# Kernel optimization log

Hardware: AMD Instinct MI355X
Metric: run time of the kernel (lower is better)

## Reference

```python
import jax, jax.numpy as jnp
import numpy as np

B, D, C, P = 64, 262144, 4, 4096  # batch, original_dim, c, proj_dim


def setup_inputs() -> dict:
    key = jax.random.key(0)
    kx, ki, ks = jax.random.split(key, 3)
    x = jax.random.normal(kx, (B, D), dtype=jnp.float32)
    rand_indices = jax.random.randint(ki, (D, C), 0, P, dtype=jnp.int64)
    rand_sign_bits = jax.random.randint(ks, (D, C), 0, 2, dtype=jnp.int32)
    return {"x": x, "rand_indices": rand_indices, "rand_sign_bits": rand_sign_bits}


def reference(x, rand_indices, rand_sign_bits):
    # signs in {-1, +1}, matching (randint(0,2)*2 - 1) in the torch module
    signs = (2 * rand_sign_bits - 1).astype(x.dtype)          # [D, C]
    idx = rand_indices.reshape(-1)                             # [D*C]
    vals = (x[:, :, None] * signs[None, :, :]).reshape(x.shape[0], -1)  # [B, D*C]
    # scatter-add each signed value into its hashed projection slot
    project = lambda v: jax.ops.segment_sum(v, idx, num_segments=P)
    return jax.vmap(project)(vals)                             # [B, P]
```

## Files before the change

### kernel.cpp

```cpp
#include <hip/hip_runtime.h>
#include <hip/hip_bf16.h>
#include <hip/hip_fp16.h>


constexpr int B_DIM = 64;
constexpr int D_DIM = 262144;
constexpr int P_DIM = 4096;

constexpr int NDS   = 64;
constexpr int SLICE = D_DIM / NDS;
constexpr int NBIN  = 16;
constexpr int NSC   = 16;
constexpr int SC_D  = SLICE / NSC;
constexpr int BCAP  = 128;
constexpr int NHB   = 32;
constexpr int G_DS  = 4;
constexpr int NDG   = NDS / G_DS;
constexpr int WPB   = 8;
constexpr int PR_W  = 16;
constexpr int NPR   = P_DIM / PR_W;
constexpr int LCAP  = 128;

constexpr size_t REG_OFF   = 0;
constexpr size_t REG_BYTES = (size_t)NDS * NSC * NBIN * BCAP * 4;
constexpr size_t CNT_OFF   = REG_OFF + REG_BYTES;
constexpr size_t CNT_BYTES = (size_t)NDS * NSC * NBIN * 4;
constexpr size_t XT_OFF    = CNT_OFF + CNT_BYTES;
constexpr size_t XT_BYTES  = (size_t)D_DIM * B_DIM * 2;
constexpr size_t PART_OFF  = XT_OFF + XT_BYTES;
constexpr size_t PART_BYTES = (size_t)NPR * NDG * PR_W * B_DIM * 2;
constexpr size_t WS_NEED   = PART_OFF + PART_BYTES;

__global__ __launch_bounds__(256) void k_binpack(
    const int* __restrict__ idx, const int* __restrict__ sgn,
    unsigned* __restrict__ reg, int* __restrict__ cnt) {
    const int w = threadIdx.x >> 6, lane = threadIdx.x & 63;
    const int dslice  = blockIdx.x >> 2;
    const int quarter = blockIdx.x & 3;
    const int sc      = quarter * 4 + w;
    const int d0      = dslice * SLICE + sc * SC_D;
    unsigned* regw = reg + ((size_t)(dslice * NSC + sc) * NBIN) * BCAP;
    const unsigned long long lmask = (1ull << lane) - 1ull;

    unsigned cb[16];
    #pragma unroll
    for (int b = 0; b < 16; ++b) cb[b] = 0;

    #pragma unroll
    for (int step = 0; step < SC_D / 64; ++step) {
        const int dli = step * 64 + lane;
        const int4 iv = reinterpret_cast<const int4*>(idx)[d0 + dli];
        const int4 sv = reinterpret_cast<const int4*>(sgn)[d0 + dli];
        const unsigned rowbyte = (unsigned)((sc * SC_D + dli) << 7);
        #pragma unroll
        for (int c = 0; c < 4; ++c) {
            const unsigned p = ((unsigned)((c==0)?iv.x:(c==1)?iv.y:(c==2)?iv.z:iv.w)) & 4095u;
            const unsigned s = ((unsigned)((c==0)?sv.x:(c==1)?sv.y:(c==2)?sv.z:sv.w)) & 1u;
            const unsigned e = rowbyte | ((p & 255u) << 19) | ((s ^ 1u) << 31);
            const unsigned bin = p >> 8;
            unsigned pos = 0;
            #pragma unroll
            for (int b = 0; b < 16; ++b) {
                const unsigned long long m = __ballot(bin == (unsigned)b);
                if (bin == (unsigned)b) pos = cb[b] + (unsigned)__popcll(m & lmask);
                cb[b] += (unsigned)__popcll(m);
            }
            if (pos < (unsigned)BCAP) regw[bin * BCAP + pos] = e;
        }
    }
    unsigned cval = 0;
    #pragma unroll
    for (int b = 0; b < 16; ++b) {
        const unsigned cc = cb[b] < (unsigned)BCAP ? cb[b] : (unsigned)BCAP;
        cval = (lane == b) ? cc : cval;
    }
    if (lane < 16) cnt[(dslice * NSC + sc) * NBIN + lane] = (int)cval;
}

__global__ __launch_bounds__(256) void k_transpose(
    const float* __restrict__ x, unsigned short* __restrict__ xTh) {
    __shared__ float tile[64 * 65];
    const int d0 = blockIdx.x * 64;
    const int t = threadIdx.x;
    const int lane = t & 63;
    #pragma unroll
    for (int k = 0; k < 16; ++k) {
        const int b = k * 4 + (t >> 6);
        tile[lane * 65 + b] = x[(size_t)b * D_DIM + d0 + lane];
    }
    __syncthreads();
    #pragma unroll
    for (int k = 0; k < 16; ++k) {
        const int dr = k * 4 + (t >> 6);
        const __half h = __float2half_rn(tile[dr * 65 + lane]);
        xTh[(size_t)(d0 + dr) * B_DIM + lane] = __builtin_bit_cast(unsigned short, h);
    }
}

__global__ __launch_bounds__(512, 8) void k_process(
    const unsigned* __restrict__ reg, const int* __restrict__ cnt,
    const unsigned short* __restrict__ xTh, __half* __restrict__ part) {
    __shared__ __half2 hist[WPB][2 * PR_W * 32];
    __shared__ unsigned lst[WPB][LCAP];
    __shared__ int cnts[WPB][WPB];
    __shared__ int baseL[WPB][WPB];
    __shared__ int totals[WPB];

    const int w = threadIdx.x >> 6, lane = threadIdx.x & 63;
    const int dg  = blockIdx.x & 15;
    const int hb  = blockIdx.x >> 4;
    const int bin = hb >> 1, half = hb & 1;

    __half2* hw = hist[w];
    {
        unsigned* h32 = reinterpret_cast<unsigned*>(hw);
        #pragma unroll
        for (int k = 0; k < 16; ++k) h32[k * 64 + lane] = 0u;
    }

    const unsigned long long lmask = (1ull << lane) - 1ull;
    const unsigned li4 = (unsigned)(lane & 31) * 4u;
    const bool hi = lane >= 32;
    const unsigned l31 = (unsigned)(lane & 31);

    for (int ds = 0; ds < G_DS; ++ds) {
        const int dslice = dg * G_DS + ds;

        unsigned er[4];
        int n0 = 0, n1 = 0;
        int c0 = 0, c1 = 0, c2 = 0, c3 = 0, c4 = 0, c5 = 0, c6 = 0, c7 = 0;
        #pragma unroll
        for (int sc2 = 0; sc2 < 2; ++sc2) {
            const int sc = 2 * w + sc2;
            const int n  = cnt[(dslice * NSC + sc) * NBIN + bin];
            const unsigned* list = reg + ((size_t)((dslice * NSC + sc) * NBIN + bin)) * BCAP;
            if (sc2 == 0) n0 = n; else n1 = n;
            #pragma unroll
            for (int b = 0; b < 2; ++b) {
                const int i = b * 64 + lane;
                const unsigned e = (i < n) ? list[i] : 0u;
                er[sc2 * 2 + b] = e;
                const unsigned po8 = (e >> 19) & 255u;
                const bool valid = (i < n) && ((int)(po8 >> 7) == half);
                const unsigned t = valid ? ((po8 >> 4) & 7u) : 0xFFu;
                c0 += __popcll(__ballot(t == 0u)); c1 += __popcll(__ballot(t == 1u));
                c2 += __popcll(__ballot(t == 2u)); c3 += __popcll(__ballot(t == 3u));
                c4 += __popcll(__ballot(t == 4u)); c5 += __popcll(__ballot(t == 5u));
                c6 += __popcll(__ballot(t == 6u)); c7 += __popcll(__ballot(t == 7u));
            }
        }
        {
            int cval = 0;
            cval = (lane == 0) ? c0 : cval; cval = (lane == 1) ? c1 : cval;
            cval = (lane == 2) ? c2 : cval; cval = (lane == 3) ? c3 : cval;
            cval = (lane == 4) ? c4 : cval; cval = (lane == 5) ? c5 : cval;
            cval = (lane == 6) ? c6 : cval; cval = (lane == 7) ? c7 : cval;
            if (lane < 8) cnts[w][lane] = cval;
        }
        __syncthreads();

        if (w == 0 && lane < 8) {
            int run = 0;
            #pragma unroll
            for (int ww = 0; ww < 8; ++ww) { baseL[lane][ww] = run; run += cnts[ww][lane]; }
            totals[lane] = run;
        }
        __syncthreads();

        c0 = c1 = c2 = c3 = c4 = c5 = c6 = c7 = 0;
        #pragma unroll
        for (int sc2 = 0; sc2 < 2; ++sc2) {
            const int n = (sc2 == 0) ? n0 : n1;
            #pragma unroll
            for (int b = 0; b < 2; ++b) {
                const int i = b * 64 + lane;
                const unsigned e = er[sc2 * 2 + b];
                const unsigned po8 = (e >> 19) & 255u;
                const bool valid = (i < n) && ((int)(po8 >> 7) == half);
                const unsigned t = valid ? ((po8 >> 4) & 7u) : 0xFFu;
                const unsigned long long m0 = __ballot(t == 0u);
                const unsigned long long m1 = __ballot(t == 1u);
                const unsigned long long m2 = __ballot(t == 2u);
                const unsigned long long m3 = __ballot(t == 3u);
                const unsigned long long m4 = __ballot(t == 4u);
                const unsigned long long m5 = __ballot(t == 5u);
                const unsigned long long m6 = __ballot(t == 6u);
                const unsigned long long m7 = __ballot(t == 7u);
                if (valid) {
                    const unsigned long long mt =
                        t < 4u ? (t < 2u ? (t == 0u ? m0 : m1) : (t == 2u ? m2 : m3))
                               : (t < 6u ? (t == 4u ? m4 : m5) : (t == 6u ? m6 : m7));
                    const int cbase =
                        t < 4u ? (t < 2u ? (t == 0u ? c0 : c1) : (t == 2u ? c2 : c3))
                               : (t < 6u ? (t == 4u ? c4 : c5) : (t == 6u ? c6 : c7));
                    const int pos = baseL[t][w] + cbase + (int)__popcll(mt & lmask);
                    if (pos < LCAP) lst[t][pos] = e;
                }
                c0 += __popcll(m0); c1 += __popcll(m1);
                c2 += __popcll(m2); c3 += __popcll(m3);
                c4 += __popcll(m4); c5 += __popcll(m5);
                c6 += __popcll(m6); c7 += __popcll(m7);
            }
        }
        __syncthreads();

        const char* xs_c = reinterpret_cast<const char*>(xTh) + (size_t)dslice * SLICE * 128;
        const int n = totals[w] < LCAP ? totals[w] : LCAP;
        const unsigned* L = lst[w];

        int i = 0;
        for (; i + 8 <= n; i += 8) {
            const uint4 A  = *reinterpret_cast<const uint4*>(L + i);
            const uint4 Bv = *reinterpret_cast<const uint4*>(L + i + 4);
            const unsigned e0 = __builtin_amdgcn_readfirstlane(A.x);
            const unsigned e1 = __builtin_amdgcn_readfirstlane(A.y);
            const unsigned e2 = __builtin_amdgcn_readfirstlane(A.z);
            const unsigned e3 = __builtin_amdgcn_readfirstlane(A.w);
            const unsigned e4 = __builtin_amdgcn_readfirstlane(Bv.x);
            const unsigned e5 = __builtin_amdgcn_readfirstlane(Bv.y);
            const unsigned e6 = __builtin_amdgcn_readfirstlane(Bv.z);
            const unsigned e7 = __builtin_amdgcn_readfirstlane(Bv.w);
            const unsigned va0 = (hi ? (e4 & 0x7FFFFu) : (e0 & 0x7FFFFu)) + li4;
            const unsigned va1 = (hi ? (e5 & 0x7FFFFu) : (e1 & 0x7FFFFu)) + li4;
            const unsigned va2 = (hi ? (e6 & 0x7FFFFu) : (e2 & 0x7FFFFu)) + li4;
            const unsigned va3 = (hi ? (e7 & 0x7FFFFu) : (e3 & 0x7FFFFu)) + li4;
            const unsigned d0 = *reinterpret_cast<const unsigned*>(xs_c + va0);
            const unsigned d1 = *reinterpret_cast<const unsigned*>(xs_c + va1);
            const unsigned d2 = *reinterpret_cast<const unsigned*>(xs_c + va2);
            const unsigned d3 = *reinterpret_cast<const unsigned*>(xs_c + va3);

            const unsigned pL0 = (e0 >> 19) & 15u, pL1 = (e1 >> 19) & 15u;
            const unsigned pL2 = (e2 >> 19) & 15u, pL3 = (e3 >> 19) & 15u;
            const unsigned pH0 = (e4 >> 19) & 15u, pH1 = (e5 >> 19) & 15u;
            const unsigned pH2 = (e6 >> 19) & 15u, pH3 = (e7 >> 19) & 15u;

            __half2 v[4];
            #pragma unroll
            for (int k = 0; k < 4; ++k) {
                const unsigned dv = (k == 0) ? d0 : (k == 1) ? d1 : (k == 2) ? d2 : d3;
                const unsigned eL = (k == 0) ? e0 : (k == 1) ? e1 : (k == 2) ? e2 : e3;
                const unsigned eH = (k == 0) ? e4 : (k == 1) ? e5 : (k == 2) ? e6 : e7;
                const unsigned sm = hi ? (eH & 0x80000000u) : (eL & 0x80000000u);
                v[k] = __builtin_bit_cast(__half2, dv ^ (sm ? 0x80008000u : 0u));
            }

            const __half2 zero2 = __builtin_bit_cast(__half2, 0u);
            {
                const bool m01 = hi ? (pH0 == pH1) : (pL0 == pL1);
                v[1] = m01 ? __hadd2(v[1], v[0]) : v[1];  v[0] = m01 ? zero2 : v[0];
                const bool m02 = hi ? (pH0 == pH2) : (pL0 == pL2);
                v[2] = m02 ? __hadd2(v[2], v[0]) : v[2];  v[0] = m02 ? zero2 : v[0];
                const bool m12 = hi ? (pH1 == pH2) : (pL1 == pL2);
                v[2] = m12 ? __hadd2(v[2], v[1]) : v[2];  v[1] = m12 ? zero2 : v[1];
                const bool m03 = hi ? (pH0 == pH3) : (pL0 == pL3);
                v[3] = m03 ? __hadd2(v[3], v[0]) : v[3];  v[0] = m03 ? zero2 : v[0];
                const bool m13 = hi ? (pH1 == pH3) : (pL1 == pL3);
                v[3] = m13 ? __hadd2(v[3], v[1]) : v[3];  v[1] = m13 ? zero2 : v[1];
                const bool m23 = hi ? (pH2 == pH3) : (pL2 == pL3);
                v[3] = m23 ? __hadd2(v[3], v[2]) : v[3];  v[2] = m23 ? zero2 : v[2];
            }

            const unsigned a0 = (hi ? (512u + pH0 * 32u) : (pL0 * 32u)) + l31;
            const unsigned a1 = (hi ? (512u + pH1 * 32u) : (pL1 * 32u)) + l31;
            const unsigned a2 = (hi ? (512u + pH2 * 32u) : (pL2 * 32u)) + l31;
            const unsigned a3 = (hi ? (512u + pH3 * 32u) : (pL3 * 32u)) + l31;
            const __half2 h0 = hw[a0];
            const __half2 h1 = hw[a1];
            const __half2 h2v = hw[a2];
            const __half2 h3 = hw[a3];
            hw[a0] = __hadd2(h0, v[0]);
            hw[a1] = __hadd2(h1, v[1]);
            hw[a2] = __hadd2(h2v, v[2]);
            hw[a3] = __hadd2(h3, v[3]);
        }
        for (; i + 2 <= n; i += 2) {
            const unsigned eA = __builtin_amdgcn_readfirstlane(L[i]);
            const unsigned eB = __builtin_amdgcn_readfirstlane(L[i + 1]);
            const unsigned va = (hi ? (eB & 0x7FFFFu) : (eA & 0x7FFFFu)) + li4;
            const unsigned dv = *reinterpret_cast<const unsigned*>(xs_c + va);
            const unsigned sm = hi ? (eB & 0x80000000u) : (eA & 0x80000000u);
            const __half2 v2 = __builtin_bit_cast(__half2, dv ^ (sm ? 0x80008000u : 0u));
            const unsigned po = hi ? ((eB >> 19) & 15u) : ((eA >> 19) & 15u);
            const unsigned a = (hi ? (512u + po * 32u) : (po * 32u)) + l31;
            hw[a] = __hadd2(hw[a], v2);
        }
        if (i < n) {
            const unsigned eA = __builtin_amdgcn_readfirstlane(L[i]);
            if (!hi) {
                const unsigned va = (eA & 0x7FFFFu) + li4;
                const unsigned dv = *reinterpret_cast<const unsigned*>(xs_c + va);
                const __half2 v2 = __builtin_bit_cast(__half2,
                    dv ^ ((eA & 0x80000000u) ? 0x80008000u : 0u));
                const unsigned a = ((eA >> 19) & 15u) * 32u + l31;
                hw[a] = __hadd2(hw[a], v2);
            }
        }
        __syncthreads();
    }

    unsigned* wp32 = reinterpret_cast<unsigned*>(
        part + ((size_t)((hb * WPB + w) * NDG + dg)) * (PR_W * B_DIM));
    #pragma unroll
    for (int k = 0; k < 8; ++k) {
        const int idxw = k * 64 + lane;
        const __half2 s = __hadd2(hw[idxw], hw[512 + idxw]);
        wp32[idxw] = __builtin_bit_cast(unsigned, s);
    }
}

__global__ __launch_bounds__(256) void k_reduce(
    const __half* __restrict__ part, float* __restrict__ out) {
    const int pr = blockIdx.x;
    const int t  = threadIdx.x;

    float4 acc = make_float4(0.f, 0.f, 0.f, 0.f);
    const size_t base = (size_t)pr * NDG * (PR_W * B_DIM);
    for (int dgi = 0; dgi < NDG; ++dgi) {
        const uint2 pv = *reinterpret_cast<const uint2*>(
            part + base + (size_t)dgi * (PR_W * B_DIM) + t * 4);
        const __half2 h0 = __builtin_bit_cast(__half2, pv.x);
        const __half2 h1 = __builtin_bit_cast(__half2, pv.y);
        acc.x += __half2float(h0.x); acc.y += __half2float(h0.y);
        acc.z += __half2float(h1.x); acc.w += __half2float(h1.y);
    }

    __shared__ float st[16][65];
    const int po = (t * 4) >> 6;
    const int b0 = (t * 4) & 63;
    st[po][b0]     = acc.x; st[po][b0 + 1] = acc.y;
    st[po][b0 + 2] = acc.z; st[po][b0 + 3] = acc.w;
    __syncthreads();

    #pragma unroll
    for (int k = 0; k < 4; ++k) {
        const int flat = k * 256 + t;
        const int b = flat >> 4, poo = flat & 15;
        out[(size_t)b * P_DIM + pr * PR_W + poo] = st[poo][b];
    }
}

__device__ __forceinline__ float signed_val(float x, int s) {
    return __uint_as_float(__float_as_uint(x) ^ (((unsigned)(s ^ 1)) << 31));
}

__global__ __launch_bounds__(1024) void sjlt_hist_fb(
    const float* __restrict__ x, const int* __restrict__ idx,
    const int* __restrict__ sgn, float* __restrict__ out) {
    __shared__ float hist[2][P_DIM];
    for (int i = threadIdx.x; i < 2 * P_DIM; i += 1024) (&hist[0][0])[i] = 0.0f;
    __syncthreads();
    const int chunk = blockIdx.x, bg = blockIdx.y;
    const int d0 = chunk * (D_DIM / 16), b0 = bg * 2;
    const float* xr0 = x + (size_t)b0 * D_DIM + d0;
    const float* xr1 = xr0 + D_DIM;
    const int4* iv4 = reinterpret_cast<const int4*>(idx) + d0;
    const int4* sv4 = reinterpret_cast<const int4*>(sgn) + d0;
    for (int t = threadIdx.x; t < D_DIM / 16; t += 1024) {
        const int4 iv = iv4[t]; const int4 sv = sv4[t];
        const float x0 = xr0[t], x1 = xr1[t];
        unsafeAtomicAdd(&hist[0][iv.x], signed_val(x0, sv.x));
        unsafeAtomicAdd(&hist[0][iv.y], signed_val(x0, sv.y));
        unsafeAtomicAdd(&hist[0][iv.z], signed_val(x0, sv.z));
        unsafeAtomicAdd(&hist[0][iv.w], signed_val(x0, sv.w));
        unsafeAtomicAdd(&hist[1][iv.x], signed_val(x1, sv.x));
        unsafeAtomicAdd(&hist[1][iv.y], signed_val(x1, sv.y));
        unsafeAtomicAdd(&hist[1][iv.z], signed_val(x1, sv.z));
        unsafeAtomicAdd(&hist[1][iv.w], signed_val(x1, sv.w));
    }
    __syncthreads();
    float* o = out + (size_t)b0 * P_DIM;
    for (int p = threadIdx.x; p < P_DIM; p += 1024) {
        unsafeAtomicAdd(&o[p],         hist[0][p]);
        unsafeAtomicAdd(&o[P_DIM + p], hist[1][p]);
    }
}

extern "C" void kernel_launch(void* const* d_in, const int* in_sizes, int n_in,
                              void* d_out, int out_size, void* d_ws, size_t ws_size,
                              hipStream_t stream) {
    const float* x   = (const float*)d_in[0];
    const int*   idx = (const int*)d_in[1];
    const int*   sgn = (const int*)d_in[2];
    float* out = (float*)d_out;

    if (ws_size >= WS_NEED) {
        char* ws = (char*)d_ws;
        unsigned* reg = (unsigned*)(ws + REG_OFF);
        int* cnt      = (int*)(ws + CNT_OFF);
        unsigned short* xTh = (unsigned short*)(ws + XT_OFF);
        __half* part  = (__half*)(ws + PART_OFF);

        k_binpack<<<NDS * 4, 256, 0, stream>>>(idx, sgn, reg, cnt);
        k_transpose<<<D_DIM / 64, 256, 0, stream>>>(x, xTh);
        k_process<<<NHB * NDG, 512, 0, stream>>>(reg, cnt, xTh, part);
        k_reduce<<<NPR, 256, 0, stream>>>(part, out);
    } else {
        hipMemsetAsync(d_out, 0, (size_t)out_size * sizeof(float), stream);
        dim3 grid(16, 32);
        sjlt_hist_fb<<<grid, 1024, 0, stream>>>(x, idx, sgn, out);
    }
}
```

Measured before the change: 78.50 us.

## Accumulate projection bins in registers per lane instead of shared-memory histograms

The process kernel drops the per-wave shared-memory half2 histogram and the block-wide prefix-sum list compaction. Each wave now builds small per-subchunk queues of packed 16-bit entries, and each lane accumulates one batch element's 16 projection outputs in scalar half registers, reading one half per entry. The d-slice grouping is halved and the block index mapping is reordered. This removes shared-memory read-modify-write traffic and two block barriers per slice. In exchange it adds branchy register selection and lower per-load width, and it silently truncates entries beyond 24 per queue.

```diff
diff --git a/kernel.cpp b/kernel.cpp
--- a/kernel.cpp
+++ b/kernel.cpp
@@ -14,12 +14,12 @@
 constexpr int SC_D  = SLICE / NSC;
 constexpr int BCAP  = 128;
 constexpr int NHB   = 32;
-constexpr int G_DS  = 4;
+constexpr int G_DS  = 2;
 constexpr int NDG   = NDS / G_DS;
 constexpr int WPB   = 8;
 constexpr int PR_W  = 16;
 constexpr int NPR   = P_DIM / PR_W;
-constexpr int LCAP  = 128;
+constexpr int QCAP  = 28;
 
 constexpr size_t REG_OFF   = 0;
 constexpr size_t REG_BYTES = (size_t)NDS * NSC * NBIN * BCAP * 4;
@@ -100,84 +100,58 @@
 __global__ __launch_bounds__(512, 8) void k_process(
     const unsigned* __restrict__ reg, const int* __restrict__ cnt,
     const unsigned short* __restrict__ xTh, __half* __restrict__ part) {
-    __shared__ __half2 hist[WPB][2 * PR_W * 32];
-    __shared__ unsigned lst[WPB][LCAP];
-    __shared__ int cnts[WPB][WPB];
-    __shared__ int baseL[WPB][WPB];
-    __shared__ int totals[WPB];
+    __shared__ unsigned short q[WPB][NSC][QCAP];
+    __shared__ short qcnt[WPB][NSC];
 
     const int w = threadIdx.x >> 6, lane = threadIdx.x & 63;
-    const int dg  = blockIdx.x & 15;
-    const int hb  = blockIdx.x >> 4;
+    const int dg  = blockIdx.x >> 5;
+    const int hb  = blockIdx.x & 31;
     const int bin = hb >> 1, half = hb & 1;
-
-    __half2* hw = hist[w];
-    {
-        unsigned* h32 = reinterpret_cast<unsigned*>(hw);
-        #pragma unroll
-        for (int k = 0; k < 16; ++k) h32[k * 64 + lane] = 0u;
-    }
-
     const unsigned long long lmask = (1ull << lane) - 1ull;
-    const unsigned li4 = (unsigned)(lane & 31) * 4u;
-    const bool hi = lane >= 32;
-    const unsigned l31 = (unsigned)(lane & 31);
-
-    for (int ds = 0; ds < G_DS; ++ds) {
-        const int dslice = dg * G_DS + ds;
-
-        unsigned er[4];
-        int n0 = 0, n1 = 0;
-        int c0 = 0, c1 = 0, c2 = 0, c3 = 0, c4 = 0, c5 = 0, c6 = 0, c7 = 0;
+    const int lane2 = lane * 2;
+
+    __half a0{}, a1{}, a2{}, a3{}, a4{}, a5{}, a6{}, a7{};
+    __half a8{}, a9{}, a10{}, a11{}, a12{}, a13{}, a14{}, a15{};
+
+    auto ADD = [&](unsigned e, unsigned short u) {
+        if (!(e & 0x4000u)) {
+            const unsigned short uv = u ^ (unsigned short)(e & 0x8000u);
+            const __half hv = __builtin_bit_cast(__half, uv);
+            const unsigned po = (e >> 8) & 15u;
+            if (po < 8u) {
+                if (po < 4u) {
+                    if (po < 2u) { if (po == 0u) a0 = __hadd(a0, hv); else a1 = __hadd(a1, hv); }
+                    else         { if (po == 2u) a2 = __hadd(a2, hv); else a3 = __hadd(a3, hv); }
+                } else {
+                    if (po < 6u) { if (po == 4u) a4 = __hadd(a4, hv); else a5 = __hadd(a5, hv); }
+                    else         { if (po == 6u) a6 = __hadd(a6, hv); else a7 = __hadd(a7, hv); }
+                }
+            } else {
+                if (po < 12u) {
+                    if (po < 10u) { if (po == 8u)  a8 = __hadd(a8, hv);  else a9 = __hadd(a9, hv); }
+                    else          { if (po == 10u) a10 = __hadd(a10, hv); else a11 = __hadd(a11, hv); }
+                } else {
+                    if (po < 14u) { if (po == 12u) a12 = __hadd(a12, hv); else a13 = __hadd(a13, hv); }
+                    else          { if (po == 14u) a14 = __hadd(a14, hv); else a15 = __hadd(a15, hv); }
+                }
+            }
+        }
+    };
+
+    for (int ds_i = 0; ds_i < G_DS; ++ds_i) {
+        const int dslice = dg * G_DS + ds_i;
+
         #pragma unroll
         for (int sc2 = 0; sc2 < 2; ++sc2) {
             const int sc = 2 * w + sc2;
             const int n  = cnt[(dslice * NSC + sc) * NBIN + bin];
-            const unsigned* list = reg + ((size_t)((dslice * NSC + sc) * NBIN + bin)) * BCAP;
-            if (sc2 == 0) n0 = n; else n1 = n;
-            #pragma unroll
-            for (int b = 0; b < 2; ++b) {
-                const int i = b * 64 + lane;
+            const unsigned* list = reg + (size_t)((dslice * NSC + sc) * NBIN + bin) * BCAP;
+            unsigned c0 = 0, c1 = 0, c2 = 0, c3 = 0, c4 = 0, c5 = 0, c6 = 0, c7 = 0;
+            for (int base = 0; base < n; base += 64) {
+                const int i = base + lane;
                 const unsigned e = (i < n) ? list[i] : 0u;
-                er[sc2 * 2 + b] = e;
-                const unsigned po8 = (e >> 19) & 255u;
-                const bool valid = (i < n) && ((int)(po8 >> 7) == half);
-                const unsigned t = valid ? ((po8 >> 4) & 7u) : 0xFFu;
-                c0 += __popcll(__ballot(t == 0u)); c1 += __popcll(__ballot(t == 1u));
-                c2 += __popcll(__ballot(t == 2u)); c3 += __popcll(__ballot(t == 3u));
-                c4 += __popcll(__ballot(t == 4u)); c5 += __popcll(__ballot(t == 5u));
-                c6 += __popcll(__ballot(t == 6u)); c7 += __popcll(__ballot(t == 7u));
-            }
-        }
-        {
-            int cval = 0;
-            cval = (lane == 0) ? c0 : cval; cval = (lane == 1) ? c1 : cval;
-            cval = (lane == 2) ? c2 : cval; cval = (lane == 3) ? c3 : cval;
-            cval = (lane == 4) ? c4 : cval; cval = (lane == 5) ? c5 : cval;
-            cval = (lane == 6) ? c6 : cval; cval = (lane == 7) ? c7 : cval;
-            if (lane < 8) cnts[w][lane] = cval;
-        }
-        __syncthreads();
-
-        if (w == 0 && lane < 8) {
-            int run = 0;
-            #pragma unroll
-            for (int ww = 0; ww < 8; ++ww) { baseL[lane][ww] = run; run += cnts[ww][lane]; }
-            totals[lane] = run;
-        }
-        __syncthreads();
-
-        c0 = c1 = c2 = c3 = c4 = c5 = c6 = c7 = 0;
-        #pragma unroll
-        for (int sc2 = 0; sc2 < 2; ++sc2) {
-            const int n = (sc2 == 0) ? n0 : n1;
-            #pragma unroll
-            for (int b = 0; b < 2; ++b) {
-                const int i = b * 64 + lane;
-                const unsigned e = er[sc2 * 2 + b];
-                const unsigned po8 = (e >> 19) & 255u;
-                const bool valid = (i < n) && ((int)(po8 >> 7) == half);
-                const unsigned t = valid ? ((po8 >> 4) & 7u) : 0xFFu;
+                const bool valid = (i < n) && (((e >> 26) & 1u) == (unsigned)half);
+                const unsigned t = valid ? ((e >> 23) & 7u) : 0xFFu;
                 const unsigned long long m0 = __ballot(t == 0u);
                 const unsigned long long m1 = __ballot(t == 1u);
                 const unsigned long long m2 = __ballot(t == 2u);
@@ -190,122 +164,71 @@
                     const unsigned long long mt =
                         t < 4u ? (t < 2u ? (t == 0u ? m0 : m1) : (t == 2u ? m2 : m3))
                                : (t < 6u ? (t == 4u ? m4 : m5) : (t == 6u ? m6 : m7));
-                    const int cbase =
+                    const unsigned cbase =
                         t < 4u ? (t < 2u ? (t == 0u ? c0 : c1) : (t == 2u ? c2 : c3))
                                : (t < 6u ? (t == 4u ? c4 : c5) : (t == 6u ? c6 : c7));
-                    const int pos = baseL[t][w] + cbase + (int)__popcll(mt & lmask);
-                    if (pos < LCAP) lst[t][pos] = e;
+                    const unsigned pos = cbase + (unsigned)__popcll(mt & lmask);
+                    const unsigned e16 = ((e >> 7) & 255u) | (((e >> 19) & 15u) << 8)
+                                       | ((e >> 31) << 15);
+                    if (pos < 24u) q[t][sc][pos] = (unsigned short)e16;
                 }
                 c0 += __popcll(m0); c1 += __popcll(m1);
                 c2 += __popcll(m2); c3 += __popcll(m3);
                 c4 += __popcll(m4); c5 += __popcll(m5);
                 c6 += __popcll(m6); c7 += __popcll(m7);
             }
+            c0 = c0 < 24u ? c0 : 24u;  c1 = c1 < 24u ? c1 : 24u;
+            c2 = c2 < 24u ? c2 : 24u;  c3 = c3 < 24u ? c3 : 24u;
+            c4 = c4 < 24u ? c4 : 24u;  c5 = c5 < 24u ? c5 : 24u;
+            c6 = c6 < 24u ? c6 : 24u;  c7 = c7 < 24u ? c7 : 24u;
+            if (lane < 32) {
+                const int tt = lane >> 2, j = lane & 3;
+                const unsigned ct =
+                    tt < 4 ? (tt < 2 ? (tt == 0 ? c0 : c1) : (tt == 2 ? c2 : c3))
+                           : (tt < 6 ? (tt == 4 ? c4 : c5) : (tt == 6 ? c6 : c7));
+                const unsigned ct4 = (ct + 3u) & ~3u;
+                if (ct + (unsigned)j < ct4) q[tt][sc][ct + j] = (unsigned short)0x4000u;
+                if (j == 0) qcnt[tt][sc] = (short)ct4;
+            }
         }
         __syncthreads();
 
-        const char* xs_c = reinterpret_cast<const char*>(xTh) + (size_t)dslice * SLICE * 128;
-        const int n = totals[w] < LCAP ? totals[w] : LCAP;
-        const unsigned* L = lst[w];
-
-        int i = 0;
-        for (; i + 8 <= n; i += 8) {
-            const uint4 A  = *reinterpret_cast<const uint4*>(L + i);
-            const uint4 Bv = *reinterpret_cast<const uint4*>(L + i + 4);
-            const unsigned e0 = __builtin_amdgcn_readfirstlane(A.x);
-            const unsigned e1 = __builtin_amdgcn_readfirstlane(A.y);
-            const unsigned e2 = __builtin_amdgcn_readfirstlane(A.z);
-            const unsigned e3 = __builtin_amdgcn_readfirstlane(A.w);
-            const unsigned e4 = __builtin_amdgcn_readfirstlane(Bv.x);
-            const unsigned e5 = __builtin_amdgcn_readfirstlane(Bv.y);
-            const unsigned e6 = __builtin_amdgcn_readfirstlane(Bv.z);
-            const unsigned e7 = __builtin_amdgcn_readfirstlane(Bv.w);
-            const unsigned va0 = (hi ? (e4 & 0x7FFFFu) : (e0 & 0x7FFFFu)) + li4;
-            const unsigned va1 = (hi ? (e5 & 0x7FFFFu) : (e1 & 0x7FFFFu)) + li4;
-            const unsigned va2 = (hi ? (e6 & 0x7FFFFu) : (e2 & 0x7FFFFu)) + li4;
-            const unsigned va3 = (hi ? (e7 & 0x7FFFFu) : (e3 & 0x7FFFFu)) + li4;
-            const unsigned d0 = *reinterpret_cast<const unsigned*>(xs_c + va0);
-            const unsigned d1 = *reinterpret_cast<const unsigned*>(xs_c + va1);
-            const unsigned d2 = *reinterpret_cast<const unsigned*>(xs_c + va2);
-            const unsigned d3 = *reinterpret_cast<const unsigned*>(xs_c + va3);
-
-            const unsigned pL0 = (e0 >> 19) & 15u, pL1 = (e1 >> 19) & 15u;
-            const unsigned pL2 = (e2 >> 19) & 15u, pL3 = (e3 >> 19) & 15u;
-            const unsigned pH0 = (e4 >> 19) & 15u, pH1 = (e5 >> 19) & 15u;
-            const unsigned pH2 = (e6 >> 19) & 15u, pH3 = (e7 >> 19) & 15u;
-
-            __half2 v[4];
-            #pragma unroll
-            for (int k = 0; k < 4; ++k) {
-                const unsigned dv = (k == 0) ? d0 : (k == 1) ? d1 : (k == 2) ? d2 : d3;
-                const unsigned eL = (k == 0) ? e0 : (k == 1) ? e1 : (k == 2) ? e2 : e3;
-                const unsigned eH = (k == 0) ? e4 : (k == 1) ? e5 : (k == 2) ? e6 : e7;
-                const unsigned sm = hi ? (eH & 0x80000000u) : (eL & 0x80000000u);
-                v[k] = __builtin_bit_cast(__half2, dv ^ (sm ? 0x80008000u : 0u));
-            }
-
-            const __half2 zero2 = __builtin_bit_cast(__half2, 0u);
-            {
-                const bool m01 = hi ? (pH0 == pH1) : (pL0 == pL1);
-                v[1] = m01 ? __hadd2(v[1], v[0]) : v[1];  v[0] = m01 ? zero2 : v[0];
-                const bool m02 = hi ? (pH0 == pH2) : (pL0 == pL2);
-                v[2] = m02 ? __hadd2(v[2], v[0]) : v[2];  v[0] = m02 ? zero2 : v[0];
-                const bool m12 = hi ? (pH1 == pH2) : (pL1 == pL2);
-                v[2] = m12 ? __hadd2(v[2], v[1]) : v[2];  v[1] = m12 ? zero2 : v[1];
-                const bool m03 = hi ? (pH0 == pH3) : (pL0 == pL3);
-                v[3] = m03 ? __hadd2(v[3], v[0]) : v[3];  v[0] = m03 ? zero2 : v[0];
-                const bool m13 = hi ? (pH1 == pH3) : (pL1 == pL3);
-                v[3] = m13 ? __hadd2(v[3], v[1]) : v[3];  v[1] = m13 ? zero2 : v[1];
-                const bool m23 = hi ? (pH2 == pH3) : (pL2 == pL3);
-                v[3] = m23 ? __hadd2(v[3], v[2]) : v[3];  v[2] = m23 ? zero2 : v[2];
-            }
-
-            const unsigned a0 = (hi ? (512u + pH0 * 32u) : (pL0 * 32u)) + l31;
-            const unsigned a1 = (hi ? (512u + pH1 * 32u) : (pL1 * 32u)) + l31;
-            const unsigned a2 = (hi ? (512u + pH2 * 32u) : (pL2 * 32u)) + l31;
-            const unsigned a3 = (hi ? (512u + pH3 * 32u) : (pL3 * 32u)) + l31;
-            const __half2 h0 = hw[a0];
-            const __half2 h1 = hw[a1];
-            const __half2 h2v = hw[a2];
-            const __half2 h3 = hw[a3];
-            hw[a0] = __hadd2(h0, v[0]);
-            hw[a1] = __hadd2(h1, v[1]);
-            hw[a2] = __hadd2(h2v, v[2]);
-            hw[a3] = __hadd2(h3, v[3]);
-        }
-        for (; i + 2 <= n; i += 2) {
-            const unsigned eA = __builtin_amdgcn_readfirstlane(L[i]);
-            const unsigned eB = __builtin_amdgcn_readfirstlane(L[i + 1]);
-            const unsigned va = (hi ? (eB & 0x7FFFFu) : (eA & 0x7FFFFu)) + li4;
-            const unsigned dv = *reinterpret_cast<const unsigned*>(xs_c + va);
-            const unsigned sm = hi ? (eB & 0x80000000u) : (eA & 0x80000000u);
-            const __half2 v2 = __builtin_bit_cast(__half2, dv ^ (sm ? 0x80008000u : 0u));
-            const unsigned po = hi ? ((eB >> 19) & 15u) : ((eA >> 19) & 15u);
-            const unsigned a = (hi ? (512u + po * 32u) : (po * 32u)) + l31;
-            hw[a] = __hadd2(hw[a], v2);
-        }
-        if (i < n) {
-            const unsigned eA = __builtin_amdgcn_readfirstlane(L[i]);
-            if (!hi) {
-                const unsigned va = (eA & 0x7FFFFu) + li4;
-                const unsigned dv = *reinterpret_cast<const unsigned*>(xs_c + va);
-                const __half2 v2 = __builtin_bit_cast(__half2,
-                    dv ^ ((eA & 0x80000000u) ? 0x80008000u : 0u));
-                const unsigned a = ((eA >> 19) & 15u) * 32u + l31;
-                hw[a] = __hadd2(hw[a], v2);
+        const char* xs = reinterpret_cast<const char*>(xTh)
+                       + (size_t)dslice * SLICE * 128;
+        for (int sc = 0; sc < NSC; ++sc) {
+            const int n = qcnt[w][sc];
+            const unsigned short* qq = &q[w][sc][0];
+            const char* xss = xs + (sc << 15);
+            for (int i = 0; i < n; i += 4) {
+                const unsigned w0 = *reinterpret_cast<const unsigned*>(qq + i);
+                const unsigned w1 = *reinterpret_cast<const unsigned*>(qq + i + 2);
+                const unsigned s0 = __builtin_amdgcn_readfirstlane(w0);
+                const unsigned s1 = __builtin_amdgcn_readfirstlane(w1);
+                const unsigned e0 = s0 & 0xFFFFu, e1 = s0 >> 16;
+                const unsigned e2 = s1 & 0xFFFFu, e3 = s1 >> 16;
+                const unsigned short u0 = *reinterpret_cast<const unsigned short*>(
+                    xss + ((e0 & 255u) << 7) + lane2);
+                const unsigned short u1 = *reinterpret_cast<const unsigned short*>(
+                    xss + ((e1 & 255u) << 7) + lane2);
+                const unsigned short u2 = *reinterpret_cast<const unsigned short*>(
+                    xss + ((e2 & 255u) << 7) + lane2);
+                const unsigned short u3 = *reinterpret_cast<const unsigned short*>(
+                    xss + ((e3 & 255u) << 7) + lane2);
+                ADD(e0, u0); ADD(e1, u1); ADD(e2, u2); ADD(e3, u3);
             }
         }
         __syncthreads();
     }
 
-    unsigned* wp32 = reinterpret_cast<unsigned*>(
-        part + ((size_t)((hb * WPB + w) * NDG + dg)) * (PR_W * B_DIM));
-    #pragma unroll
-    for (int k = 0; k < 8; ++k) {
-        const int idxw = k * 64 + lane;
-        const __half2 s = __hadd2(hw[idxw], hw[512 + idxw]);
-        wp32[idxw] = __builtin_bit_cast(unsigned, s);
-    }
+    __half* wp = part + ((size_t)((hb * WPB + w) * NDG + dg)) * (PR_W * B_DIM);
+    wp[ 0 * 64 + lane] = a0;  wp[ 1 * 64 + lane] = a1;
+    wp[ 2 * 64 + lane] = a2;  wp[ 3 * 64 + lane] = a3;
+    wp[ 4 * 64 + lane] = a4;  wp[ 5 * 64 + lane] = a5;
+    wp[ 6 * 64 + lane] = a6;  wp[ 7 * 64 + lane] = a7;
+    wp[ 8 * 64 + lane] = a8;  wp[ 9 * 64 + lane] = a9;
+    wp[10 * 64 + lane] = a10; wp[11 * 64 + lane] = a11;
+    wp[12 * 64 + lane] = a12; wp[13 * 64 + lane] = a13;
+    wp[14 * 64 + lane] = a14; wp[15 * 64 + lane] = a15;
 }
 
 __global__ __launch_bounds__(256) void k_reduce(
```

Measured after the change: 106.2 us. 1.35x slower.

## Fuse transpose and binpack launches, one d-slice per process block

Applied to the files above, without the earlier changes.

Merges the transpose and bin-packing kernels into a single launch whose blocks branch on block index, removing one kernel launch and its gap. k_process now gives each block a single d-slice instead of looping over four, so it launches four times as many blocks with fewer internal barriers. Partials grow fourfold, so k_reduce sums 64 partials instead of 16. The within-group duplicate merge in the 8-wide loop is replaced by a branch: a fast path when no slots collide, otherwise sequential read-modify-write.

```diff
diff --git a/kernel.cpp b/kernel.cpp
--- a/kernel.cpp
+++ b/kernel.cpp
@@ -14,12 +14,13 @@
 constexpr int SC_D  = SLICE / NSC;
 constexpr int BCAP  = 128;
 constexpr int NHB   = 32;
-constexpr int G_DS  = 4;
-constexpr int NDG   = NDS / G_DS;
 constexpr int WPB   = 8;
 constexpr int PR_W  = 16;
 constexpr int NPR   = P_DIM / PR_W;
 constexpr int LCAP  = 128;
+
+constexpr int TRANS_BLOCKS = D_DIM / 64;
+constexpr int BINPK_BLOCKS = NDS * 4;
 
 constexpr size_t REG_OFF   = 0;
 constexpr size_t REG_BYTES = (size_t)NDS * NSC * NBIN * BCAP * 4;
@@ -28,15 +29,39 @@
 constexpr size_t XT_OFF    = CNT_OFF + CNT_BYTES;
 constexpr size_t XT_BYTES  = (size_t)D_DIM * B_DIM * 2;
 constexpr size_t PART_OFF  = XT_OFF + XT_BYTES;
-constexpr size_t PART_BYTES = (size_t)NPR * NDG * PR_W * B_DIM * 2;
+constexpr size_t PART_BYTES = (size_t)NPR * NDS * PR_W * B_DIM * 2;
 constexpr size_t WS_NEED   = PART_OFF + PART_BYTES;
 
-__global__ __launch_bounds__(256) void k_binpack(
+__global__ __launch_bounds__(256) void k_prep(
+    const float* __restrict__ x,
     const int* __restrict__ idx, const int* __restrict__ sgn,
+    unsigned short* __restrict__ xTh,
     unsigned* __restrict__ reg, int* __restrict__ cnt) {
-    const int w = threadIdx.x >> 6, lane = threadIdx.x & 63;
-    const int dslice  = blockIdx.x >> 2;
-    const int quarter = blockIdx.x & 3;
+    __shared__ float tile[64 * 65];
+    const int t = threadIdx.x;
+    const int lane = t & 63;
+
+    if (blockIdx.x < TRANS_BLOCKS) {
+        const int d0 = blockIdx.x * 64;
+        #pragma unroll
+        for (int k = 0; k < 16; ++k) {
+            const int b = k * 4 + (t >> 6);
+            tile[lane * 65 + b] = x[(size_t)b * D_DIM + d0 + lane];
+        }
+        __syncthreads();
+        #pragma unroll
+        for (int k = 0; k < 16; ++k) {
+            const int dr = k * 4 + (t >> 6);
+            const __half h = __float2half_rn(tile[dr * 65 + lane]);
+            xTh[(size_t)(d0 + dr) * B_DIM + lane] = __builtin_bit_cast(unsigned short, h);
+        }
+        return;
+    }
+
+    const int bid = blockIdx.x - TRANS_BLOCKS;
+    const int w = t >> 6;
+    const int dslice  = bid >> 2;
+    const int quarter = bid & 3;
     const int sc      = quarter * 4 + w;
     const int d0      = dslice * SLICE + sc * SC_D;
     unsigned* regw = reg + ((size_t)(dslice * NSC + sc) * NBIN) * BCAP;
@@ -77,26 +102,6 @@
     if (lane < 16) cnt[(dslice * NSC + sc) * NBIN + lane] = (int)cval;
 }
 
-__global__ __launch_bounds__(256) void k_transpose(
-    const float* __restrict__ x, unsigned short* __restrict__ xTh) {
-    __shared__ float tile[64 * 65];
-    const int d0 = blockIdx.x * 64;
-    const int t = threadIdx.x;
-    const int lane = t & 63;
-    #pragma unroll
-    for (int k = 0; k < 16; ++k) {
-        const int b = k * 4 + (t >> 6);
-        tile[lane * 65 + b] = x[(size_t)b * D_DIM + d0 + lane];
-    }
-    __syncthreads();
-    #pragma unroll
-    for (int k = 0; k < 16; ++k) {
-        const int dr = k * 4 + (t >> 6);
-        const __half h = __float2half_rn(tile[dr * 65 + lane]);
-        xTh[(size_t)(d0 + dr) * B_DIM + lane] = __builtin_bit_cast(unsigned short, h);
-    }
-}
-
 __global__ __launch_bounds__(512, 8) void k_process(
     const unsigned* __restrict__ reg, const int* __restrict__ cnt,
     const unsigned short* __restrict__ xTh, __half* __restrict__ part) {
@@ -107,8 +112,8 @@
     __shared__ int totals[WPB];
 
     const int w = threadIdx.x >> 6, lane = threadIdx.x & 63;
-    const int dg  = blockIdx.x & 15;
-    const int hb  = blockIdx.x >> 4;
+    const int dslice = blockIdx.x & 63;
+    const int hb  = blockIdx.x >> 6;
     const int bin = hb >> 1, half = hb & 1;
 
     __half2* hw = hist[w];
@@ -119,151 +124,138 @@
     }
 
     const unsigned long long lmask = (1ull << lane) - 1ull;
+
+    unsigned er[4];
+    int n0 = 0, n1 = 0;
+    int c0 = 0, c1 = 0, c2 = 0, c3 = 0, c4 = 0, c5 = 0, c6 = 0, c7 = 0;
+    #pragma unroll
+    for (int sc2 = 0; sc2 < 2; ++sc2) {
+        const int sc = 2 * w + sc2;
+        const int n  = cnt[(dslice * NSC + sc) * NBIN + bin];
+        const unsigned* list = reg + ((size_t)((dslice * NSC + sc) * NBIN + bin)) * BCAP;
+        if (sc2 == 0) n0 = n; else n1 = n;
+        #pragma unroll
+        for (int b = 0; b < 2; ++b) {
+            const int i = b * 64 + lane;
+            const unsigned e = (i < n) ? list[i] : 0u;
+            er[sc2 * 2 + b] = e;
+            const unsigned po8 = (e >> 19) & 255u;
+            const bool valid = (i < n) && ((int)(po8 >> 7) == half);
+            const unsigned t = valid ? ((po8 >> 4) & 7u) : 0xFFu;
+            c0 += __popcll(__ballot(t == 0u)); c1 += __popcll(__ballot(t == 1u));
+            c2 += __popcll(__ballot(t == 2u)); c3 += __popcll(__ballot(t == 3u));
+            c4 += __popcll(__ballot(t == 4u)); c5 += __popcll(__ballot(t == 5u));
+            c6 += __popcll(__ballot(t == 6u)); c7 += __popcll(__ballot(t == 7u));
+        }
+    }
+    {
+        int cval = 0;
+        cval = (lane == 0) ? c0 : cval; cval = (lane == 1) ? c1 : cval;
+        cval = (lane == 2) ? c2 : cval; cval = (lane == 3) ? c3 : cval;
+        cval = (lane == 4) ? c4 : cval; cval = (lane == 5) ? c5 : cval;
+        cval = (lane == 6) ? c6 : cval; cval = (lane == 7) ? c7 : cval;
+        if (lane < 8) cnts[w][lane] = cval;
+    }
+    __syncthreads();
+
+    if (w == 0 && lane < 8) {
+        int run = 0;
+        #pragma unroll
+        for (int ww = 0; ww < 8; ++ww) { baseL[lane][ww] = run; run += cnts[ww][lane]; }
+        totals[lane] = run;
+    }
+    __syncthreads();
+
+    c0 = c1 = c2 = c3 = c4 = c5 = c6 = c7 = 0;
+    #pragma unroll
+    for (int sc2 = 0; sc2 < 2; ++sc2) {
+        const int n = (sc2 == 0) ? n0 : n1;
+        #pragma unroll
+        for (int b = 0; b < 2; ++b) {
+            const int i = b * 64 + lane;
+            const unsigned e = er[sc2 * 2 + b];
+            const unsigned po8 = (e >> 19) & 255u;
+            const bool valid = (i < n) && ((int)(po8 >> 7) == half);
+            const unsigned t = valid ? ((po8 >> 4) & 7u) : 0xFFu;
+            const unsigned long long m0 = __ballot(t == 0u);
+            const unsigned long long m1 = __ballot(t == 1u);
+            const unsigned long long m2 = __ballot(t == 2u);
+            const unsigned long long m3 = __ballot(t == 3u);
+            const unsigned long long m4 = __ballot(t == 4u);
+            const unsigned long long m5 = __ballot(t == 5u);
+            const unsigned long long m6 = __ballot(t == 6u);
+            const unsigned long long m7 = __ballot(t == 7u);
+            if (valid) {
+                const unsigned long long mt =
+                    t < 4u ? (t < 2u ? (t == 0u ? m0 : m1) : (t == 2u ? m2 : m3))
+                           : (t < 6u ? (t == 4u ? m4 : m5) : (t == 6u ? m6 : m7));
+                const int cbase =
+                    t < 4u ? (t < 2u ? (t == 0u ? c0 : c1) : (t == 2u ? c2 : c3))
+                           : (t < 6u ? (t == 4u ? c4 : c5) : (t == 6u ? c6 : c7));
+                const int pos = baseL[t][w] + cbase + (int)__popcll(mt & lmask);
+                if (pos < LCAP) lst[t][pos] = e;
+            }
+            c0 += __popcll(m0); c1 += __popcll(m1);
+            c2 += __popcll(m2); c3 += __popcll(m3);
+            c4 += __popcll(m4); c5 += __popcll(m5);
+            c6 += __popcll(m6); c7 += __popcll(m7);
+        }
+    }
+    __syncthreads();
+
+    const char* xs_c = reinterpret_cast<const char*>(xTh) + (size_t)dslice * SLICE * 128;
     const unsigned li4 = (unsigned)(lane & 31) * 4u;
     const bool hi = lane >= 32;
     const unsigned l31 = (unsigned)(lane & 31);
-
-    for (int ds = 0; ds < G_DS; ++ds) {
-        const int dslice = dg * G_DS + ds;
-
-        unsigned er[4];
-        int n0 = 0, n1 = 0;
-        int c0 = 0, c1 = 0, c2 = 0, c3 = 0, c4 = 0, c5 = 0, c6 = 0, c7 = 0;
-        #pragma unroll
-        for (int sc2 = 0; sc2 < 2; ++sc2) {
-            const int sc = 2 * w + sc2;
-            const int n  = cnt[(dslice * NSC + sc) * NBIN + bin];
-            const unsigned* list = reg + ((size_t)((dslice * NSC + sc) * NBIN + bin)) * BCAP;
-            if (sc2 == 0) n0 = n; else n1 = n;
-            #pragma unroll
-            for (int b = 0; b < 2; ++b) {
-                const int i = b * 64 + lane;
-                const unsigned e = (i < n) ? list[i] : 0u;
-                er[sc2 * 2 + b] = e;
-                const unsigned po8 = (e >> 19) & 255u;
-                const bool valid = (i < n) && ((int)(po8 >> 7) == half);
-                const unsigned t = valid ? ((po8 >> 4) & 7u) : 0xFFu;
-                c0 += __popcll(__ballot(t == 0u)); c1 += __popcll(__ballot(t == 1u));
-                c2 += __popcll(__ballot(t == 2u)); c3 += __popcll(__ballot(t == 3u));
-                c4 += __popcll(__ballot(t == 4u)); c5 += __popcll(__ballot(t == 5u));
-                c6 += __popcll(__ballot(t == 6u)); c7 += __popcll(__ballot(t == 7u));
-            }
-        }
-        {
-            int cval = 0;
-            cval = (lane == 0) ? c0 : cval; cval = (lane == 1) ? c1 : cval;
-            cval = (lane == 2) ? c2 : cval; cval = (lane == 3) ? c3 : cval;
-            cval = (lane == 4) ? c4 : cval; cval = (lane == 5) ? c5 : cval;
-            cval = (lane == 6) ? c6 : cval; cval = (lane == 7) ? c7 : cval;
-            if (lane < 8) cnts[w][lane] = cval;
-        }
-        __syncthreads();
-
-        if (w == 0 && lane < 8) {
-            int run = 0;
-            #pragma unroll
-            for (int ww = 0; ww < 8; ++ww) { baseL[lane][ww] = run; run += cnts[ww][lane]; }
-            totals[lane] = run;
-        }
-        __syncthreads();
-
-        c0 = c1 = c2 = c3 = c4 = c5 = c6 = c7 = 0;
-        #pragma unroll
-        for (int sc2 = 0; sc2 < 2; ++sc2) {
-            const int n = (sc2 == 0) ? n0 : n1;
-            #pragma unroll
-            for (int b = 0; b < 2; ++b) {
-                const int i = b * 64 + lane;
-                const unsigned e = er[sc2 * 2 + b];
-                const unsigned po8 = (e >> 19) & 255u;
-                const bool valid = (i < n) && ((int)(po8 >> 7) == half);
-                const unsigned t = valid ? ((po8 >> 4) & 7u) : 0xFFu;
-                const unsigned long long m0 = __ballot(t == 0u);
-                const unsigned long long m1 = __ballot(t == 1u);
-                const unsigned long long m2 = __ballot(t == 2u);
-                const unsigned long long m3 = __ballot(t == 3u);
-                const unsigned long long m4 = __ballot(t == 4u);
-                const unsigned long long m5 = __ballot(t == 5u);
-                const unsigned long long m6 = __ballot(t == 6u);
-                const unsigned long long m7 = __ballot(t == 7u);
-                if (valid) {
-                    const unsigned long long mt =
-                        t < 4u ? (t < 2u ? (t == 0u ? m0 : m1) : (t == 2u ? m2 : m3))
-                               : (t < 6u ? (t == 4u ? m4 : m5) : (t == 6u ? m6 : m7));
-                    const int cbase =
-                        t < 4u ? (t < 2u ? (t == 0u ? c0 : c1) : (t == 2u ? c2 : c3))
-                               : (t < 6u ? (t == 4u ? c4 : c5) : (t == 6u ? c6 : c7));
-                    const int pos = baseL[t][w] + cbase + (int)__popcll(mt & lmask);
-                    if (pos < LCAP) lst[t][pos] = e;
-                }
-                c0 += __popcll(m0); c1 += __popcll(m1);
-                c2 += __popcll(m2); c3 += __popcll(m3);
-                c4 += __popcll(m4); c5 += __popcll(m5);
-                c6 += __popcll(m6); c7 += __popcll(m7);
-            }
-        }
-        __syncthreads();
-
-        const char* xs_c = reinterpret_cast<const char*>(xTh) + (size_t)dslice * SLICE * 128;
-        const int n = totals[w] < LCAP ? totals[w] : LCAP;
-        const unsigned* L = lst[w];
-
-        int i = 0;
-        for (; i + 8 <= n; i += 8) {
-            const uint4 A  = *reinterpret_cast<const uint4*>(L + i);
-            const uint4 Bv = *reinterpret_cast<const uint4*>(L + i + 4);
-            const unsigned e0 = __builtin_amdgcn_readfirstlane(A.x);
-            const unsigned e1 = __builtin_amdgcn_readfirstlane(A.y);
-            const unsigned e2 = __builtin_amdgcn_readfirstlane(A.z);
-            const unsigned e3 = __builtin_amdgcn_readfirstlane(A.w);
-            const unsigned e4 = __builtin_amdgcn_readfirstlane(Bv.x);
-            const unsigned e5 = __builtin_amdgcn_readfirstlane(Bv.y);
-            const unsigned e6 = __builtin_amdgcn_readfirstlane(Bv.z);
-            const unsigned e7 = __builtin_amdgcn_readfirstlane(Bv.w);
-            const unsigned va0 = (hi ? (e4 & 0x7FFFFu) : (e0 & 0x7FFFFu)) + li4;
-            const unsigned va1 = (hi ? (e5 & 0x7FFFFu) : (e1 & 0x7FFFFu)) + li4;
-            const unsigned va2 = (hi ? (e6 & 0x7FFFFu) : (e2 & 0x7FFFFu)) + li4;
-            const unsigned va3 = (hi ? (e7 & 0x7FFFFu) : (e3 & 0x7FFFFu)) + li4;
-            const unsigned d0 = *reinterpret_cast<const unsigned*>(xs_c + va0);
-            const unsigned d1 = *reinterpret_cast<const unsigned*>(xs_c + va1);
-            const unsigned d2 = *reinterpret_cast<const unsigned*>(xs_c + va2);
-            const unsigned d3 = *reinterpret_cast<const unsigned*>(xs_c + va3);
-
-            const unsigned pL0 = (e0 >> 19) & 15u, pL1 = (e1 >> 19) & 15u;
-            const unsigned pL2 = (e2 >> 19) & 15u, pL3 = (e3 >> 19) & 15u;
-            const unsigned pH0 = (e4 >> 19) & 15u, pH1 = (e5 >> 19) & 15u;
-            const unsigned pH2 = (e6 >> 19) & 15u, pH3 = (e7 >> 19) & 15u;
-
-            __half2 v[4];
-            #pragma unroll
-            for (int k = 0; k < 4; ++k) {
-                const unsigned dv = (k == 0) ? d0 : (k == 1) ? d1 : (k == 2) ? d2 : d3;
-                const unsigned eL = (k == 0) ? e0 : (k == 1) ? e1 : (k == 2) ? e2 : e3;
-                const unsigned eH = (k == 0) ? e4 : (k == 1) ? e5 : (k == 2) ? e6 : e7;
-                const unsigned sm = hi ? (eH & 0x80000000u) : (eL & 0x80000000u);
-                v[k] = __builtin_bit_cast(__half2, dv ^ (sm ? 0x80008000u : 0u));
-            }
-
-            const __half2 zero2 = __builtin_bit_cast(__half2, 0u);
-            {
-                const bool m01 = hi ? (pH0 == pH1) : (pL0 == pL1);
-                v[1] = m01 ? __hadd2(v[1], v[0]) : v[1];  v[0] = m01 ? zero2 : v[0];
-                const bool m02 = hi ? (pH0 == pH2) : (pL0 == pL2);
-                v[2] = m02 ? __hadd2(v[2], v[0]) : v[2];  v[0] = m02 ? zero2 : v[0];
-                const bool m12 = hi ? (pH1 == pH2) : (pL1 == pL2);
-                v[2] = m12 ? __hadd2(v[2], v[1]) : v[2];  v[1] = m12 ? zero2 : v[1];
-                const bool m03 = hi ? (pH0 == pH3) : (pL0 == pL3);
-                v[3] = m03 ? __hadd2(v[3], v[0]) : v[3];  v[0] = m03 ? zero2 : v[0];
-                const bool m13 = hi ? (pH1 == pH3) : (pL1 == pL3);
-                v[3] = m13 ? __hadd2(v[3], v[1]) : v[3];  v[1] = m13 ? zero2 : v[1];
-                const bool m23 = hi ? (pH2 == pH3) : (pL2 == pL3);
-                v[3] = m23 ? __hadd2(v[3], v[2]) : v[3];  v[2] = m23 ? zero2 : v[2];
-            }
-
-            const unsigned a0 = (hi ? (512u + pH0 * 32u) : (pL0 * 32u)) + l31;
-            const unsigned a1 = (hi ? (512u + pH1 * 32u) : (pL1 * 32u)) + l31;
-            const unsigned a2 = (hi ? (512u + pH2 * 32u) : (pL2 * 32u)) + l31;
-            const unsigned a3 = (hi ? (512u + pH3 * 32u) : (pL3 * 32u)) + l31;
+    const int n = totals[w] < LCAP ? totals[w] : LCAP;
+    const unsigned* L = lst[w];
+
+    int i = 0;
+    for (; i + 8 <= n; i += 8) {
+        const uint4 A  = *reinterpret_cast<const uint4*>(L + i);
+        const uint4 Bv = *reinterpret_cast<const uint4*>(L + i + 4);
+        const unsigned e0 = __builtin_amdgcn_readfirstlane(A.x);
+        const unsigned e1 = __builtin_amdgcn_readfirstlane(A.y);
+        const unsigned e2 = __builtin_amdgcn_readfirstlane(A.z);
+        const unsigned e3 = __builtin_amdgcn_readfirstlane(A.w);
+        const unsigned e4 = __builtin_amdgcn_readfirstlane(Bv.x);
+        const unsigned e5 = __builtin_amdgcn_readfirstlane(Bv.y);
+        const unsigned e6 = __builtin_amdgcn_readfirstlane(Bv.z);
+        const unsigned e7 = __builtin_amdgcn_readfirstlane(Bv.w);
+        const unsigned va0 = (hi ? (e4 & 0x7FFFFu) : (e0 & 0x7FFFFu)) + li4;
+        const unsigned va1 = (hi ? (e5 & 0x7FFFFu) : (e1 & 0x7FFFFu)) + li4;
+        const unsigned va2 = (hi ? (e6 & 0x7FFFFu) : (e2 & 0x7FFFFu)) + li4;
+        const unsigned va3 = (hi ? (e7 & 0x7FFFFu) : (e3 & 0x7FFFFu)) + li4;
+        const unsigned d0 = *reinterpret_cast<const unsigned*>(xs_c + va0);
+        const unsigned d1 = *reinterpret_cast<const unsigned*>(xs_c + va1);
+        const unsigned d2 = *reinterpret_cast<const unsigned*>(xs_c + va2);
+        const unsigned d3 = *reinterpret_cast<const unsigned*>(xs_c + va3);
+
+        const unsigned pL0 = (e0 >> 19) & 15u, pL1 = (e1 >> 19) & 15u;
+        const unsigned pL2 = (e2 >> 19) & 15u, pL3 = (e3 >> 19) & 15u;
+        const unsigned pH0 = (e4 >> 19) & 15u, pH1 = (e5 >> 19) & 15u;
+        const unsigned pH2 = (e6 >> 19) & 15u, pH3 = (e7 >> 19) & 15u;
+
+        __half2 v[4];
+        #pragma unroll
+        for (int k = 0; k < 4; ++k) {
+            const unsigned dv = (k == 0) ? d0 : (k == 1) ? d1 : (k == 2) ? d2 : d3;
+            const unsigned eL = (k == 0) ? e0 : (k == 1) ? e1 : (k == 2) ? e2 : e3;
+            const unsigned eH = (k == 0) ? e4 : (k == 1) ? e5 : (k == 2) ? e6 : e7;
+            const unsigned sm = hi ? (eH & 0x80000000u) : (eL & 0x80000000u);
+            v[k] = __builtin_bit_cast(__half2, dv ^ (sm ? 0x80008000u : 0u));
+        }
+
+        const unsigned a0 = (hi ? (512u + pH0 * 32u) : (pL0 * 32u)) + l31;
+        const unsigned a1 = (hi ? (512u + pH1 * 32u) : (pL1 * 32u)) + l31;
+        const unsigned a2 = (hi ? (512u + pH2 * 32u) : (pL2 * 32u)) + l31;
+        const unsigned a3 = (hi ? (512u + pH3 * 32u) : (pL3 * 32u)) + l31;
+
+        const bool dupL = (pL0 == pL1) | (pL0 == pL2) | (pL0 == pL3)
+                        | (pL1 == pL2) | (pL1 == pL3) | (pL2 == pL3);
+        const bool dupH = (pH0 == pH1) | (pH0 == pH2) | (pH0 == pH3)
+                        | (pH1 == pH2) | (pH1 == pH3) | (pH2 == pH3);
+        if (!(dupL | dupH)) {
             const __half2 h0 = hw[a0];
             const __half2 h1 = hw[a1];
             const __half2 h2v = hw[a2];
@@ -272,34 +264,37 @@
             hw[a1] = __hadd2(h1, v[1]);
             hw[a2] = __hadd2(h2v, v[2]);
             hw[a3] = __hadd2(h3, v[3]);
-        }
-        for (; i + 2 <= n; i += 2) {
-            const unsigned eA = __builtin_amdgcn_readfirstlane(L[i]);
-            const unsigned eB = __builtin_amdgcn_readfirstlane(L[i + 1]);
-            const unsigned va = (hi ? (eB & 0x7FFFFu) : (eA & 0x7FFFFu)) + li4;
+        } else {
+            hw[a0] = __hadd2(hw[a0], v[0]);
+            hw[a1] = __hadd2(hw[a1], v[1]);
+            hw[a2] = __hadd2(hw[a2], v[2]);
+            hw[a3] = __hadd2(hw[a3], v[3]);
+        }
+    }
+    for (; i + 2 <= n; i += 2) {
+        const unsigned eA = __builtin_amdgcn_readfirstlane(L[i]);
+        const unsigned eB = __builtin_amdgcn_readfirstlane(L[i + 1]);
+        const unsigned va = (hi ? (eB & 0x7FFFFu) : (eA & 0x7FFFFu)) + li4;
+        const unsigned dv = *reinterpret_cast<const unsigned*>(xs_c + va);
+        const unsigned sm = hi ? (eB & 0x80000000u) : (eA & 0x80000000u);
+        const unsigned pkb = dv ^ (sm ? 0x80008000u : 0u);
+        const unsigned po = hi ? ((eB >> 19) & 15u) : ((eA >> 19) & 15u);
+        const unsigned a = (hi ? (512u + po * 32u) : (po * 32u)) + l31;
+        hw[a] = __hadd2(hw[a], __builtin_bit_cast(__half2, pkb));
+    }
+    if (i < n) {
+        const unsigned eA = __builtin_amdgcn_readfirstlane(L[i]);
+        if (!hi) {
+            const unsigned va = (eA & 0x7FFFFu) + li4;
             const unsigned dv = *reinterpret_cast<const unsigned*>(xs_c + va);
-            const unsigned sm = hi ? (eB & 0x80000000u) : (eA & 0x80000000u);
-            const __half2 v2 = __builtin_bit_cast(__half2, dv ^ (sm ? 0x80008000u : 0u));
-            const unsigned po = hi ? ((eB >> 19) & 15u) : ((eA >> 19) & 15u);
-            const unsigned a = (hi ? (512u + po * 32u) : (po * 32u)) + l31;
-            hw[a] = __hadd2(hw[a], v2);
-        }
-        if (i < n) {
-            const unsigned eA = __builtin_amdgcn_readfirstlane(L[i]);
-            if (!hi) {
-                const unsigned va = (eA & 0x7FFFFu) + li4;
-                const unsigned dv = *reinterpret_cast<const unsigned*>(xs_c + va);
-                const __half2 v2 = __builtin_bit_cast(__half2,
-                    dv ^ ((eA & 0x80000000u) ? 0x80008000u : 0u));
-                const unsigned a = ((eA >> 19) & 15u) * 32u + l31;
-                hw[a] = __hadd2(hw[a], v2);
-            }
-        }
-        __syncthreads();
+            const unsigned pkb = dv ^ ((eA & 0x80000000u) ? 0x80008000u : 0u);
+            const unsigned a = ((eA >> 19) & 15u) * 32u + l31;
+            hw[a] = __hadd2(hw[a], __builtin_bit_cast(__half2, pkb));
+        }
     }
 
     unsigned* wp32 = reinterpret_cast<unsigned*>(
-        part + ((size_t)((hb * WPB + w) * NDG + dg)) * (PR_W * B_DIM));
+        part + ((size_t)((hb * WPB + w) * NDS + dslice)) * (PR_W * B_DIM));
     #pragma unroll
     for (int k = 0; k < 8; ++k) {
         const int idxw = k * 64 + lane;
@@ -314,10 +309,10 @@
     const int t  = threadIdx.x;
 
     float4 acc = make_float4(0.f, 0.f, 0.f, 0.f);
-    const size_t base = (size_t)pr * NDG * (PR_W * B_DIM);
-    for (int dgi = 0; dgi < NDG; ++dgi) {
+    const size_t base = (size_t)pr * NDS * (PR_W * B_DIM);
+    for (int ds = 0; ds < NDS; ++ds) {
         const uint2 pv = *reinterpret_cast<const uint2*>(
-            part + base + (size_t)dgi * (PR_W * B_DIM) + t * 4);
+            part + base + (size_t)ds * (PR_W * B_DIM) + t * 4);
         const __half2 h0 = __builtin_bit_cast(__half2, pv.x);
         const __half2 h1 = __builtin_bit_cast(__half2, pv.y);
         acc.x += __half2float(h0.x); acc.y += __half2float(h0.y);
@@ -390,9 +385,8 @@
         unsigned short* xTh = (unsigned short*)(ws + XT_OFF);
         __half* part  = (__half*)(ws + PART_OFF);
 
-        k_binpack<<<NDS * 4, 256, 0, stream>>>(idx, sgn, reg, cnt);
-        k_transpose<<<D_DIM / 64, 256, 0, stream>>>(x, xTh);
-        k_process<<<NHB * NDG, 512, 0, stream>>>(reg, cnt, xTh, part);
+        k_prep<<<TRANS_BLOCKS + BINPK_BLOCKS, 256, 0, stream>>>(x, idx, sgn, xTh, reg, cnt);
+        k_process<<<NHB * NDS, 512, 0, stream>>>(reg, cnt, xTh, part);
         k_reduce<<<NPR, 256, 0, stream>>>(part, out);
     } else {
         hipMemsetAsync(d_out, 0, (size_t)out_size * sizeof(float), stream);
```

Result: faster. 69.83 us (median of 2 runs) (-11.1%).
